# Kernel optimization log

Hardware: AMD Instinct MI355X
Metric: run time of the kernel (lower is better)

## Reference

```python
import jax, jax.numpy as jnp
import numpy as np
import math

B, T, D = 16, 2048, 512
W = 12  # window_size


def setup_inputs() -> dict:
    key = jax.random.key(0)
    ks = jax.random.split(key, 5)
    s = 1.0 / math.sqrt(D)
    x = jax.random.normal(ks[0], (B, T, D), dtype=jnp.float32)
    w_ih = jax.random.uniform(ks[1], (3 * D, D), jnp.float32, -s, s)
    w_hh = jax.random.uniform(ks[2], (3 * D, D), jnp.float32, -s, s)
    b_ih = jax.random.uniform(ks[3], (3 * D,), jnp.float32, -s, s)
    b_hh = jax.random.uniform(ks[4], (3 * D,), jnp.float32, -s, s)
    return {"x": x, "w_ih": w_ih, "w_hh": w_hh, "b_ih": b_ih, "b_hh": b_hh}


def reference(x, w_ih, w_hh, b_ih, b_hh):
    b, t, d = x.shape
    # QK^T scores, scaled
    scores = jnp.einsum('btd,bsd->bts', x, x) / math.sqrt(d)
    # local band mask: allowed where |i-j| <= window_size - 1 (local_ws = 2*W)
    idx = jnp.arange(t)
    band = jnp.abs(idx[:, None] - idx[None, :]) <= (W - 1)
    scores = jnp.where(band[None], scores, -1e9)
    # top-k indices per (batch, timestep), sorted ascending (indices are detached)
    ids = jax.lax.top_k(scores, W)[1]            # [B, T, W]
    ids = jnp.sort(ids, axis=-1)
    # eval-mode temporal subsampling: T//4 evenly spaced timesteps (static)
    tids = np.sort(np.linspace(0, t - 1, t // 4).astype(np.int32))
    ids_sel = ids[:, tids, :]                    # [B, Tq, W]
    # gather local windows: feature[b, j, w] = x[b, ids_sel[b, j, w]]
    feature = jnp.take_along_axis(x[:, None, :, :], ids_sel[..., None], axis=2)  # [B, Tq, W, D]
    tq = feature.shape[1]
    seq = feature.reshape(-1, W, d).transpose(1, 0, 2)  # [W, B*Tq, D]

    def gru_step(h, xt):
        gi = xt @ w_ih.T + b_ih
        gh = h @ w_hh.T + b_hh
        i_r, i_z, i_n = jnp.split(gi, 3, axis=-1)
        h_r, h_z, h_n = jnp.split(gh, 3, axis=-1)
        r = jax.nn.sigmoid(i_r + h_r)
        z = jax.nn.sigmoid(i_z + h_z)
        n = jnp.tanh(i_n + r * h_n)
        h = (1.0 - z) * n + z * h
        return h, None

    h0 = jnp.zeros((seq.shape[1], d), dtype=x.dtype)
    h_final, _ = jax.lax.scan(gru_step, h0, seq)
    return h_final.reshape(b, tq, d)
```

## Files before the change

### kernel.cpp

```cpp
#include <hip/hip_runtime.h>
#include <math.h>

#define BB 16
#define TT 2048
#define DD 512
#define WW 12
#define TQ 512
#define NROWS (BB * TQ)

typedef _Float16 f16;
typedef __attribute__((ext_vector_type(8))) _Float16 f16x8;
typedef __attribute__((ext_vector_type(4))) _Float16 f16x4;
typedef __attribute__((ext_vector_type(4))) float f32x4;

#define MFMA16(a, b, c) __builtin_amdgcn_mfma_f32_16x16x32_f16((a), (b), (c), 0, 0, 0)

#define WS_IDS  0u
#define WS_W16  (512u * 1024u)
#define WS_H16  (4u * 1024u * 1024u)
#define WS_GI   (12u * 1024u * 1024u)
#define WS_X16  (108ull * 1024ull * 1024ull)
#define WS_NEED_X16 (140ull * 1024ull * 1024ull)

#define SEL_BLOCKS 2048
#define W_BLOCKS   1536
#define X_BLOCKS   16384

__device__ __forceinline__ float fsigm(float v) { return 1.0f / (1.0f + __expf(-v)); }
__device__ __forceinline__ float ftanh(float v) {
    float a = fabsf(v);
    float t = __expf(-2.0f * a);
    float r = (1.0f - t) / (1.0f + t);
    return copysignf(r, v);
}

__device__ __forceinline__ f16x8 cvt8(float4 a, float4 b) {
    f16x8 r;
    r[0] = (_Float16)a.x; r[1] = (_Float16)a.y; r[2] = (_Float16)a.z; r[3] = (_Float16)a.w;
    r[4] = (_Float16)b.x; r[5] = (_Float16)b.y; r[6] = (_Float16)b.z; r[7] = (_Float16)b.w;
    return r;
}

__global__ __launch_bounds__(256, 4) void prep_kernel(
    const float* __restrict__ x, int* __restrict__ ids,
    const float* __restrict__ wi, const float* __restrict__ wh,
    f16* __restrict__ w16, f16* __restrict__ x16, int has_x16)
{
    const int bid = blockIdx.x;
    const int tid = threadIdx.x;

    if (bid >= SEL_BLOCKS) {
        int rel = bid - SEL_BLOCKS;
        if (rel < W_BLOCKS) {
            const int PER = 3 * DD * DD / 4;
            int i = rel * 256 + tid;
            float4 v;
            if (i < PER) v = ((const float4*)wi)[i];
            else         v = ((const float4*)wh)[i - PER];
            f16x4 o;
            o[0] = (_Float16)v.x; o[1] = (_Float16)v.y; o[2] = (_Float16)v.z; o[3] = (_Float16)v.w;
            *(f16x4*)(w16 + (size_t)i * 4) = o;
        } else {
            int j = (rel - W_BLOCKS) * 256 + tid;
            float4 v = ((const float4*)x)[j];
            f16x4 o;
            o[0] = (_Float16)v.x; o[1] = (_Float16)v.y; o[2] = (_Float16)v.z; o[3] = (_Float16)v.w;
            *(f16x4*)(x16 + (size_t)j * 4) = o;
        }
        return;
    }

    const int wid = tid >> 6, lane = tid & 63;
    const int swz = (bid & 7) * 256 + (bid >> 3);
    const int n = swz * 4 + wid;
    const int b = n >> 9, qi = n & 511;

    int t = (qi == TQ - 1) ? (TT - 1)
          : (int)((double)qi * ((double)(TT - 1) / (double)(TQ - 1)));
    int j0 = t - (WW - 1); if (j0 < 0) j0 = 0;
    int j1 = t + (WW - 1); if (j1 > TT - 1) j1 = TT - 1;
    const int ncand = j1 - j0 + 1;

    const int c = lane & 3, i = lane >> 2;
    const float* qrow = x + ((size_t)b * TT + t) * DD + i * 4;

    float4 q[8];
#pragma unroll
    for (int it = 0; it < 8; ++it) q[it] = *(const float4*)(qrow + it * 64);

    double sv[6];
#pragma unroll
    for (int r = 0; r < 6; ++r) {
        int cc = r * 4 + c;
        int jr = j0 + cc; if (jr > j1) jr = j1;
        const float* krow = x + ((size_t)b * TT + jr) * DD + i * 4;
        double s0 = 0.0, s1 = 0.0;
#pragma unroll
        for (int it = 0; it < 8; ++it) {
            float4 kv = *(const float4*)(krow + it * 64);
            s0 = fma((double)q[it].x, (double)kv.x, s0);
            s1 = fma((double)q[it].y, (double)kv.y, s1);
            s0 = fma((double)q[it].z, (double)kv.z, s0);
            s1 = fma((double)q[it].w, (double)kv.w, s1);
        }
        sv[r] = s0 + s1;
    }

#pragma unroll
    for (int r = 0; r < 6; ++r) {
        double v = sv[r];
        v += __shfl_xor(v, 4);
        v += __shfl_xor(v, 8);
        v += __shfl_xor(v, 16);
        v += __shfl_xor(v, 32);
        sv[r] = v;
    }

    const int rr = lane >> 2;
    double sj = sv[0];
    sj = (rr == 1) ? sv[1] : sj;
    sj = (rr == 2) ? sv[2] : sj;
    sj = (rr == 3) ? sv[3] : sj;
    sj = (rr == 4) ? sv[4] : sj;
    sj = (rr == 5) ? sv[5] : sj;
    bool valid = lane < ncand;
    if (!valid) sj = -1.0e300;

    int rank = 0;
    for (int kk = 0; kk < 2 * WW - 1; ++kk) {
        if (kk >= ncand) break;
        double bs = __shfl(sj, kk);
        rank += (bs > sj || (bs == sj && kk < lane)) ? 1 : 0;
    }
    bool sel = valid && (rank < WW);
    unsigned long long m = __ballot(sel);
    if (sel) {
        int pos = __popcll(m & ((1ull << lane) - 1ull));
        ids[(size_t)n * WW + pos] = j0 + lane;
    }
}

template<bool X16PATH>
__global__ __launch_bounds__(256, 2) void gi_gemm_kernel(
    const float* __restrict__ x,
    const f16* __restrict__ x16,
    const f16* __restrict__ w16,
    const float* __restrict__ b_ih,
    f16* __restrict__ gi)
{
    __shared__ __align__(16) char sB[2][16 * 1024];
    __shared__ __align__(16) char sX[2][16 * 1024];

    const int tid = threadIdx.x;
    const int lane = tid & 63, wid = tid >> 6;
    const int wm = wid >> 1, wn = wid & 1;
    const int l15 = lane & 15, lhi = lane >> 4;
    const int bid = blockIdx.x;
    const int xcd = bid & 7, idx = bid >> 3;
    const int rb = xcd * 32 + idx / 12;
    const int cb = idx % 12;
    const int row0 = rb * 128, c0 = cb * 128;

    const int slot = lane & 3, lc = lane >> 2;
    const f16* bsrc[4]; int bdst[4];
#pragma unroll
    for (int ii = 0; ii < 4; ++ii) {
        int ch = wid * 4 + ii;
        int half = ch >> 3, cg = ch & 7;
        int col = cg * 16 + lc;
        bsrc[ii] = w16 + ((size_t)(c0 + col) * 512 + half * 32
                          + (size_t)((slot ^ ((col >> 1) & 3)) * 8));
        bdst[ii] = half * 8192 + cg * 1024;
    }

    const f16* x16src[4]; int x16dst[4];
    const float* xps[2]; int xdst[2];
    if (X16PATH) {
        const int xrl = lane >> 2, xslot = lane & 3;
        const int xswz = (xslot ^ ((xrl >> 1) & 3)) * 8;
#pragma unroll
        for (int ii = 0; ii < 4; ++ii) {
            int ch2 = wid * 4 + ii;
            int hh = ch2 >> 3, ch = ch2 & 7;
            x16src[ii] = x16 + ((size_t)(row0 + ch * 16 + xrl) * 512 + hh * 32 + xswz);
            x16dst[ii] = hh * 8192 + ch * 1024;
        }
    } else {
#pragma unroll
        for (int seg = 0; seg < 2; ++seg) {
            int row = seg * 64 + (tid >> 2);
            int chunk = (tid & 3) ^ ((row >> 1) & 3);
            xps[seg] = x + (size_t)(row0 + row) * DD + chunk * 8;
            xdst[seg] = seg * 4096 + tid * 16;
        }
    }

    const int swzo = (lhi ^ ((l15 >> 1) & 3)) * 16;
    const int aBase = (wm * 64 + l15) * 64 + swzo;
    const int bBase = (wn * 64 + l15) * 64 + swzo;

    f32x4 acc[4][4];
#pragma unroll
    for (int mf = 0; mf < 4; ++mf)
#pragma unroll
        for (int nf = 0; nf < 4; ++nf) { f32x4 z = {0.f,0.f,0.f,0.f}; acc[mf][nf] = z; }

    {
#pragma unroll
        for (int ii = 0; ii < 4; ++ii)
            __builtin_amdgcn_global_load_lds(
                (const __attribute__((address_space(1))) unsigned*)bsrc[ii],
                (__attribute__((address_space(3))) unsigned*)(&sB[0][0] + bdst[ii]), 16, 0, 0);
        if (X16PATH) {
#pragma unroll
            for (int ii = 0; ii < 4; ++ii)
                __builtin_amdgcn_global_load_lds(
                    (const __attribute__((address_space(1))) unsigned*)x16src[ii],
                    (__attribute__((address_space(3))) unsigned*)(&sX[0][0] + x16dst[ii]), 16, 0, 0);
        } else {
#pragma unroll
            for (int seg = 0; seg < 2; ++seg)
#pragma unroll
                for (int h = 0; h < 2; ++h) {
                    float4 a0 = *(const float4*)(xps[seg] + h * 32);
                    float4 a1 = *(const float4*)(xps[seg] + h * 32 + 4);
                    *(f16x8*)(&sX[0][0] + h * 8192 + xdst[seg]) = cvt8(a0, a1);
                }
        }
    }

    int cur = 0;
    for (int ks = 0; ks < 8; ++ks) {
        asm volatile("s_waitcnt vmcnt(0)" ::: "memory");
        __syncthreads();

        const int kn = (ks + 1) * 64;
        float4 a[2][2][2];
        if (ks < 7) {
#pragma unroll
            for (int ii = 0; ii < 4; ++ii)
                __builtin_amdgcn_global_load_lds(
                    (const __attribute__((address_space(1))) unsigned*)(bsrc[ii] + kn),
                    (__attribute__((address_space(3))) unsigned*)(&sB[cur ^ 1][0] + bdst[ii]), 16, 0, 0);
            if (X16PATH) {
#pragma unroll
                for (int ii = 0; ii < 4; ++ii)
                    __builtin_amdgcn_global_load_lds(
                        (const __attribute__((address_space(1))) unsigned*)(x16src[ii] + kn),
                        (__attribute__((address_space(3))) unsigned*)(&sX[cur ^ 1][0] + x16dst[ii]), 16, 0, 0);
            } else {
#pragma unroll
                for (int seg = 0; seg < 2; ++seg)
#pragma unroll
                    for (int h = 0; h < 2; ++h) {
                        a[seg][h][0] = *(const float4*)(xps[seg] + kn + h * 32);
                        a[seg][h][1] = *(const float4*)(xps[seg] + kn + h * 32 + 4);
                    }
            }
        }

        __builtin_amdgcn_s_setprio(1);
#pragma unroll
        for (int h = 0; h < 2; ++h) {
            f16x8 ax[4];
#pragma unroll
            for (int mf = 0; mf < 4; ++mf)
                ax[mf] = *(const f16x8*)(&sX[cur][0] + h * 8192 + aBase + mf * 1024);
#pragma unroll
            for (int nf = 0; nf < 4; ++nf) {
                f16x8 Bv = *(const f16x8*)(&sB[cur][0] + h * 8192 + bBase + nf * 1024);
#pragma unroll
                for (int mf = 0; mf < 4; ++mf)
                    acc[mf][nf] = MFMA16(ax[mf], Bv, acc[mf][nf]);
            }
        }
        __builtin_amdgcn_s_setprio(0);

        if (!X16PATH && ks < 7) {
#pragma unroll
            for (int seg = 0; seg < 2; ++seg)
#pragma unroll
                for (int h = 0; h < 2; ++h)
                    *(f16x8*)(&sX[cur ^ 1][0] + h * 8192 + xdst[seg]) = cvt8(a[seg][h][0], a[seg][h][1]);
        }
        cur ^= 1;
    }

#pragma unroll
    for (int nf = 0; nf < 4; ++nf) {
        int col = c0 + wn * 64 + nf * 16 + l15;
        float bi = b_ih[col];
#pragma unroll
        for (int mf = 0; mf < 4; ++mf)
#pragma unroll
            for (int r = 0; r < 4; ++r) {
                int row = row0 + wm * 64 + mf * 16 + lhi * 4 + r;
                gi[(size_t)row * 1536 + col] = (f16)(acc[mf][nf][r] + bi);
            }
    }
}

__global__ __launch_bounds__(256) void step0_kernel(
    const int* __restrict__ ids, const f16* __restrict__ gi,
    const float* __restrict__ b_hh, f16* __restrict__ h16w)
{
    int g = blockIdx.x * 256 + threadIdx.x;
    int row = g >> 6;
    int c8 = (g & 63) * 8;
    int src = (row >> 9) * TT + ids[(size_t)row * WW + 0];
    const f16* gr = gi + (size_t)src * 1536 + c8;
    f16x8 vr = *(const f16x8*)(gr);
    f16x8 vz = *(const f16x8*)(gr + 512);
    f16x8 vn = *(const f16x8*)(gr + 1024);
    f16x8 out;
#pragma unroll
    for (int j = 0; j < 8; ++j) {
        int col = c8 + j;
        float R = fsigm((float)vr[j] + b_hh[col]);
        float Z = fsigm((float)vz[j] + b_hh[DD + col]);
        float N = ftanh((float)vn[j] + R * b_hh[2 * DD + col]);
        out[j] = (f16)((1.0f - Z) * N);
    }
    *(f16x8*)(h16w + (size_t)row * DD + c8) = out;
}

__global__ __launch_bounds__(256, 2) void gru_step_h_kernel(
    const int* __restrict__ ids,
    const f16* __restrict__ w16,
    const float* __restrict__ b_hh,
    const f16* __restrict__ gi,
    const f16* __restrict__ h16r,
    f16* __restrict__ h16w,
    float* __restrict__ f32w,
    int step)
{
    __shared__ __align__(16) char sB[2][24 * 1024];
    __shared__ __align__(16) char sH[2][16 * 1024];

    const int tid = threadIdx.x;
    const int lane = tid & 63, wid = tid >> 6;
    const int wm = wid >> 1, wn = wid & 1;
    const int l15 = lane & 15, lhi = lane >> 4;
    const int bid = blockIdx.x;
    const int xcd = bid & 7, idx = bid >> 3;
    const int rb = xcd * 8 + (idx & 7);
    const int cb = idx >> 3;
    const int row0 = rb * 128, c0 = cb * 64;

    const int lrow = lane >> 3, lslot = lane & 7;
    const int sswz = (lslot ^ lrow) * 8;

    const f16* bsrc[6]; int bdst[6];
#pragma unroll
    for (int ii = 0; ii < 6; ++ii) {
        int ch = wid * 6 + ii;
        int gate = ch >> 3, cg = ch & 7;
        int col = cg * 8 + lrow;
        bsrc[ii] = w16 + ((size_t)(1536 + gate * 512 + c0 + col) * 512 + sswz);
        bdst[ii] = gate * 8192 + cg * 1024 + lrow * 128 + lslot * 16;
    }
    const f16* hsrc[4]; int hdst[4];
#pragma unroll
    for (int ii = 0; ii < 4; ++ii) {
        int ch = wid * 4 + ii;
        int hrow = ch * 8 + lrow;
        hsrc[ii] = h16r + ((size_t)(row0 + hrow) * 512 + sswz);
        hdst[ii] = ch * 1024 + lrow * 128 + lslot * 16;
    }

    const int rowrd = wm * 64 + l15;
    const int colrd = wn * 32 + l15;
    int aOff[4][2], bOff[2][2];
#pragma unroll
    for (int mf = 0; mf < 4; ++mf)
#pragma unroll
        for (int h = 0; h < 2; ++h) {
            int rr2 = rowrd + mf * 16;
            aOff[mf][h] = rr2 * 128 + ((((h << 2) | lhi) ^ (rr2 & 7)) << 4);
        }
#pragma unroll
    for (int nf = 0; nf < 2; ++nf)
#pragma unroll
        for (int h = 0; h < 2; ++h) {
            int cc = colrd + nf * 16;
            bOff[nf][h] = cc * 128 + ((((h << 2) | lhi) ^ (cc & 7)) << 4);
        }

    f32x4 accR[4][2], accZ[4][2], accHN[4][2];
#pragma unroll
    for (int mf = 0; mf < 4; ++mf)
#pragma unroll
        for (int nf = 0; nf < 2; ++nf) {
            f32x4 z = {0.f, 0.f, 0.f, 0.f};
            accR[mf][nf] = z; accZ[mf][nf] = z; accHN[mf][nf] = z;
        }

#pragma unroll
    for (int ii = 0; ii < 6; ++ii)
        __builtin_amdgcn_global_load_lds(
            (const __attribute__((address_space(1))) unsigned*)bsrc[ii],
            (__attribute__((address_space(3))) unsigned*)(&sB[0][0] + bdst[ii]), 16, 0, 0);
#pragma unroll
    for (int ii = 0; ii < 4; ++ii)
        __builtin_amdgcn_global_load_lds(
            (const __attribute__((address_space(1))) unsigned*)hsrc[ii],
            (__attribute__((address_space(3))) unsigned*)(&sH[0][0] + hdst[ii]), 16, 0, 0);

    int cur = 0;
    for (int ks = 0; ks < 8; ++ks) {
        asm volatile("s_waitcnt vmcnt(0)" ::: "memory");
        __syncthreads();

        const int kn = (ks + 1) * 64;
        if (ks < 7) {
#pragma unroll
            for (int ii = 0; ii < 6; ++ii)
                __builtin_amdgcn_global_load_lds(
                    (const __attribute__((address_space(1))) unsigned*)(bsrc[ii] + kn),
                    (__attribute__((address_space(3))) unsigned*)(&sB[cur ^ 1][0] + bdst[ii]), 16, 0, 0);
#pragma unroll
            for (int ii = 0; ii < 4; ++ii)
                __builtin_amdgcn_global_load_lds(
                    (const __attribute__((address_space(1))) unsigned*)(hsrc[ii] + kn),
                    (__attribute__((address_space(3))) unsigned*)(&sH[cur ^ 1][0] + hdst[ii]), 16, 0, 0);
        }

        __builtin_amdgcn_s_setprio(1);
#pragma unroll
        for (int h = 0; h < 2; ++h) {
            f16x8 ah[4];
#pragma unroll
            for (int mf = 0; mf < 4; ++mf)
                ah[mf] = *(const f16x8*)(&sH[cur][0] + aOff[mf][h]);
#pragma unroll
            for (int nf = 0; nf < 2; ++nf) {
                const char* bb = &sB[cur][0] + bOff[nf][h];
                f16x8 B0 = *(const f16x8*)(bb + 0 * 8192);
                f16x8 B1 = *(const f16x8*)(bb + 1 * 8192);
                f16x8 B2 = *(const f16x8*)(bb + 2 * 8192);
#pragma unroll
                for (int mf = 0; mf < 4; ++mf) {
                    accR[mf][nf]  = MFMA16(ah[mf], B0, accR[mf][nf]);
                    accZ[mf][nf]  = MFMA16(ah[mf], B1, accZ[mf][nf]);
                    accHN[mf][nf] = MFMA16(ah[mf], B2, accHN[mf][nf]);
                }
            }
        }
        __builtin_amdgcn_s_setprio(0);
        cur ^= 1;
    }

    float bh[2][3];
#pragma unroll
    for (int nf = 0; nf < 2; ++nf) {
        int col = c0 + wn * 32 + nf * 16 + l15;
        bh[nf][0] = b_hh[col];
        bh[nf][1] = b_hh[DD + col];
        bh[nf][2] = b_hh[2 * DD + col];
    }
#pragma unroll
    for (int mf = 0; mf < 4; ++mf) {
        float g0[2][4], g1[2][4], g2[2][4], hv[2][4];
#pragma unroll
        for (int nf = 0; nf < 2; ++nf) {
            int col = c0 + wn * 32 + nf * 16 + l15;
#pragma unroll
            for (int r = 0; r < 4; ++r) {
                int row = row0 + wm * 64 + mf * 16 + lhi * 4 + r;
                int src = (row >> 9) * TT + ids[(size_t)row * WW + step];
                const f16* gr = gi + (size_t)src * 1536 + col;
                g0[nf][r] = (float)gr[0];
                g1[nf][r] = (float)gr[512];
                g2[nf][r] = (float)gr[1024];
                hv[nf][r] = (float)h16r[(size_t)row * DD + col];
            }
        }
#pragma unroll
        for (int nf = 0; nf < 2; ++nf) {
            int col = c0 + wn * 32 + nf * 16 + l15;
#pragma unroll
            for (int r = 0; r < 4; ++r) {
                int row = row0 + wm * 64 + mf * 16 + lhi * 4 + r;
                size_t off = (size_t)row * DD + col;
                float R = fsigm(g0[nf][r] + accR[mf][nf][r] + bh[nf][0]);
                float Z = fsigm(g1[nf][r] + accZ[mf][nf][r] + bh[nf][1]);
                float N = ftanh(g2[nf][r] + R * (accHN[mf][nf][r] + bh[nf][2]));
                float res = (1.0f - Z) * N + Z * hv[nf][r];
                if (h16w) h16w[off] = (f16)res;
                if (f32w) f32w[off] = res;
            }
        }
    }
}

extern "C" void kernel_launch(void* const* d_in, const int* in_sizes, int n_in,
                              void* d_out, int out_size, void* d_ws, size_t ws_size,
                              hipStream_t stream)
{
    const float* x    = (const float*)d_in[0];
    const float* w_ih = (const float*)d_in[1];
    const float* w_hh = (const float*)d_in[2];
    const float* b_ih = (const float*)d_in[3];
    const float* b_hh = (const float*)d_in[4];

    char* ws = (char*)d_ws;
    int*  ids = (int*)(ws + WS_IDS);
    f16*  w16 = (f16*)(ws + WS_W16);
    f16*  P0  = (f16*)(ws + WS_H16);
    f16*  P1  = (f16*)d_out;
    f16*  gi  = (f16*)(ws + WS_GI);
    float* fo = (float*)d_out;

    const int has_x16 = (ws_size >= WS_NEED_X16) ? 1 : 0;
    f16* x16 = has_x16 ? (f16*)(ws + WS_X16) : nullptr;

    int prep_grid = SEL_BLOCKS + W_BLOCKS + (has_x16 ? X_BLOCKS : 0);
    prep_kernel<<<dim3(prep_grid), dim3(256), 0, stream>>>(
        x, ids, w_ih, w_hh, w16, x16, has_x16);

    if (has_x16)
        gi_gemm_kernel<true><<<dim3(3072), dim3(256), 0, stream>>>(x, x16, w16, b_ih, gi);
    else
        gi_gemm_kernel<false><<<dim3(3072), dim3(256), 0, stream>>>(x, x16, w16, b_ih, gi);

    step0_kernel<<<dim3(2048), dim3(256), 0, stream>>>(ids, gi, b_hh, P0);

    for (int s = 1; s < WW; ++s) {
        const f16* hr = (s & 1) ? P0 : P1;
        f16* hw      = (s == WW - 1) ? nullptr : ((s & 1) ? P1 : P0);
        float* fw    = (s == WW - 1) ? fo : nullptr;
        gru_step_h_kernel<<<dim3(512), dim3(256), 0, stream>>>(
            ids, w16, b_hh, gi, hr, hw, fw, s);
    }
}
```

Before: 427.8 us.

## Fuse GRU recurrent steps into one persistent cooperative kernel with per-row-block flags

Replaces the eleven separate per-step GRU kernel launches with a single cooperative persistent kernel that loops over steps. Blocks that share a 128-row block synchronise through an atomic counter, so there is no grid-wide barrier between steps. Each step's hidden state goes to its own workspace buffer, which avoids write-after-read hazards without a full barrier. The aim is to remove launch overhead and inter-kernel drain between dependent steps. In exchange it needs more workspace, adds a memset and spin-waiting, and depends on cooperative launch succeeding.

```diff
diff --git a/kernel.cpp b/kernel.cpp
--- a/kernel.cpp
+++ b/kernel.cpp
@@ -15,12 +15,16 @@
 
 #define MFMA16(a, b, c) __builtin_amdgcn_mfma_f32_16x16x32_f16((a), (b), (c), 0, 0, 0)
 
-#define WS_IDS  0u
-#define WS_W16  (512u * 1024u)
-#define WS_H16  (4u * 1024u * 1024u)
-#define WS_GI   (12u * 1024u * 1024u)
-#define WS_X16  (108ull * 1024ull * 1024ull)
-#define WS_NEED_X16 (140ull * 1024ull * 1024ull)
+#define WS_IDS   0u
+#define WS_W16   (512u * 1024u)
+#define WS_FLAGS (3584u * 1024u)
+#define WS_P0    (4u * 1024u * 1024u)
+#define WS_GI    (12u * 1024u * 1024u)
+#define WS_X16   (108ull * 1024ull * 1024ull)
+#define WS_P5    (140ull * 1024ull * 1024ull)
+#define WS_NEED_X16     (140ull * 1024ull * 1024ull)
+#define WS_NEED_PERSIST (188ull * 1024ull * 1024ull)
+#define HSZ ((size_t)NROWS * DD)
 
 #define SEL_BLOCKS 2048
 #define W_BLOCKS   1536
@@ -324,67 +328,31 @@
     *(f16x8*)(h16w + (size_t)row * DD + c8) = out;
 }
 
-__global__ __launch_bounds__(256, 2) void gru_step_h_kernel(
-    const int* __restrict__ ids,
-    const f16* __restrict__ w16,
-    const float* __restrict__ b_hh,
-    const f16* __restrict__ gi,
-    const f16* __restrict__ h16r,
-    f16* __restrict__ h16w,
-    float* __restrict__ f32w,
-    int step)
-{
-    __shared__ __align__(16) char sB[2][24 * 1024];
-    __shared__ __align__(16) char sH[2][16 * 1024];
-
-    const int tid = threadIdx.x;
-    const int lane = tid & 63, wid = tid >> 6;
-    const int wm = wid >> 1, wn = wid & 1;
-    const int l15 = lane & 15, lhi = lane >> 4;
-    const int bid = blockIdx.x;
-    const int xcd = bid & 7, idx = bid >> 3;
-    const int rb = xcd * 8 + (idx & 7);
-    const int cb = idx >> 3;
-    const int row0 = rb * 128, c0 = cb * 64;
-
+struct StepPre {
+    const f16* bsrc[6]; int bdst[6];
+    int aOff[4][2], bOff[2][2];
+    int row0, c0, wm, wn, l15, lhi, tid;
+};
+
+__device__ __forceinline__ void gru_body(
+    const StepPre& P, char (*sB)[24 * 1024], char (*sH)[16 * 1024],
+    const int* __restrict__ ids, const float* __restrict__ b_hh,
+    const f16* __restrict__ gi, const f16* __restrict__ h16r,
+    f16* __restrict__ h16w, float* __restrict__ f32w, int step)
+{
+    const int wid = P.tid >> 6;
+    const int lane = P.tid & 63;
     const int lrow = lane >> 3, lslot = lane & 7;
     const int sswz = (lslot ^ lrow) * 8;
 
-    const f16* bsrc[6]; int bdst[6];
-#pragma unroll
-    for (int ii = 0; ii < 6; ++ii) {
-        int ch = wid * 6 + ii;
-        int gate = ch >> 3, cg = ch & 7;
-        int col = cg * 8 + lrow;
-        bsrc[ii] = w16 + ((size_t)(1536 + gate * 512 + c0 + col) * 512 + sswz);
-        bdst[ii] = gate * 8192 + cg * 1024 + lrow * 128 + lslot * 16;
-    }
     const f16* hsrc[4]; int hdst[4];
 #pragma unroll
     for (int ii = 0; ii < 4; ++ii) {
         int ch = wid * 4 + ii;
         int hrow = ch * 8 + lrow;
-        hsrc[ii] = h16r + ((size_t)(row0 + hrow) * 512 + sswz);
+        hsrc[ii] = h16r + ((size_t)(P.row0 + hrow) * 512 + sswz);
         hdst[ii] = ch * 1024 + lrow * 128 + lslot * 16;
     }
-
-    const int rowrd = wm * 64 + l15;
-    const int colrd = wn * 32 + l15;
-    int aOff[4][2], bOff[2][2];
-#pragma unroll
-    for (int mf = 0; mf < 4; ++mf)
-#pragma unroll
-        for (int h = 0; h < 2; ++h) {
-            int rr2 = rowrd + mf * 16;
-            aOff[mf][h] = rr2 * 128 + ((((h << 2) | lhi) ^ (rr2 & 7)) << 4);
-        }
-#pragma unroll
-    for (int nf = 0; nf < 2; ++nf)
-#pragma unroll
-        for (int h = 0; h < 2; ++h) {
-            int cc = colrd + nf * 16;
-            bOff[nf][h] = cc * 128 + ((((h << 2) | lhi) ^ (cc & 7)) << 4);
-        }
 
     f32x4 accR[4][2], accZ[4][2], accHN[4][2];
 #pragma unroll
@@ -398,8 +366,8 @@
 #pragma unroll
     for (int ii = 0; ii < 6; ++ii)
         __builtin_amdgcn_global_load_lds(
-            (const __attribute__((address_space(1))) unsigned*)bsrc[ii],
-            (__attribute__((address_space(3))) unsigned*)(&sB[0][0] + bdst[ii]), 16, 0, 0);
+            (const __attribute__((address_space(1))) unsigned*)P.bsrc[ii],
+            (__attribute__((address_space(3))) unsigned*)(&sB[0][0] + P.bdst[ii]), 16, 0, 0);
 #pragma unroll
     for (int ii = 0; ii < 4; ++ii)
         __builtin_amdgcn_global_load_lds(
@@ -416,8 +384,8 @@
 #pragma unroll
             for (int ii = 0; ii < 6; ++ii)
                 __builtin_amdgcn_global_load_lds(
-                    (const __attribute__((address_space(1))) unsigned*)(bsrc[ii] + kn),
-                    (__attribute__((address_space(3))) unsigned*)(&sB[cur ^ 1][0] + bdst[ii]), 16, 0, 0);
+                    (const __attribute__((address_space(1))) unsigned*)(P.bsrc[ii] + kn),
+                    (__attribute__((address_space(3))) unsigned*)(&sB[cur ^ 1][0] + P.bdst[ii]), 16, 0, 0);
 #pragma unroll
             for (int ii = 0; ii < 4; ++ii)
                 __builtin_amdgcn_global_load_lds(
@@ -431,10 +399,10 @@
             f16x8 ah[4];
 #pragma unroll
             for (int mf = 0; mf < 4; ++mf)
-                ah[mf] = *(const f16x8*)(&sH[cur][0] + aOff[mf][h]);
+                ah[mf] = *(const f16x8*)(&sH[cur][0] + P.aOff[mf][h]);
 #pragma unroll
             for (int nf = 0; nf < 2; ++nf) {
-                const char* bb = &sB[cur][0] + bOff[nf][h];
+                const char* bb = &sB[cur][0] + P.bOff[nf][h];
                 f16x8 B0 = *(const f16x8*)(bb + 0 * 8192);
                 f16x8 B1 = *(const f16x8*)(bb + 1 * 8192);
                 f16x8 B2 = *(const f16x8*)(bb + 2 * 8192);
@@ -453,7 +421,7 @@
     float bh[2][3];
 #pragma unroll
     for (int nf = 0; nf < 2; ++nf) {
-        int col = c0 + wn * 32 + nf * 16 + l15;
+        int col = P.c0 + P.wn * 32 + nf * 16 + P.l15;
         bh[nf][0] = b_hh[col];
         bh[nf][1] = b_hh[DD + col];
         bh[nf][2] = b_hh[2 * DD + col];
@@ -463,10 +431,10 @@
         float g0[2][4], g1[2][4], g2[2][4], hv[2][4];
 #pragma unroll
         for (int nf = 0; nf < 2; ++nf) {
-            int col = c0 + wn * 32 + nf * 16 + l15;
+            int col = P.c0 + P.wn * 32 + nf * 16 + P.l15;
 #pragma unroll
             for (int r = 0; r < 4; ++r) {
-                int row = row0 + wm * 64 + mf * 16 + lhi * 4 + r;
+                int row = P.row0 + P.wm * 64 + mf * 16 + P.lhi * 4 + r;
                 int src = (row >> 9) * TT + ids[(size_t)row * WW + step];
                 const f16* gr = gi + (size_t)src * 1536 + col;
                 g0[nf][r] = (float)gr[0];
@@ -477,10 +445,10 @@
         }
 #pragma unroll
         for (int nf = 0; nf < 2; ++nf) {
-            int col = c0 + wn * 32 + nf * 16 + l15;
+            int col = P.c0 + P.wn * 32 + nf * 16 + P.l15;
 #pragma unroll
             for (int r = 0; r < 4; ++r) {
-                int row = row0 + wm * 64 + mf * 16 + lhi * 4 + r;
+                int row = P.row0 + P.wm * 64 + mf * 16 + P.lhi * 4 + r;
                 size_t off = (size_t)row * DD + col;
                 float R = fsigm(g0[nf][r] + accR[mf][nf][r] + bh[nf][0]);
                 float Z = fsigm(g1[nf][r] + accZ[mf][nf][r] + bh[nf][1]);
@@ -493,6 +461,110 @@
     }
 }
 
+__device__ __forceinline__ void step_pre_init(StepPre& P, const f16* w16)
+{
+    const int tid = P.tid;
+    const int lane = tid & 63, wid = tid >> 6;
+    const int lrow = lane >> 3, lslot = lane & 7;
+    const int sswz = (lslot ^ lrow) * 8;
+#pragma unroll
+    for (int ii = 0; ii < 6; ++ii) {
+        int ch = wid * 6 + ii;
+        int gate = ch >> 3, cg = ch & 7;
+        int col = cg * 8 + lrow;
+        P.bsrc[ii] = w16 + ((size_t)(1536 + gate * 512 + P.c0 + col) * 512 + sswz);
+        P.bdst[ii] = gate * 8192 + cg * 1024 + lrow * 128 + lslot * 16;
+    }
+    const int rowrd = P.wm * 64 + P.l15;
+    const int colrd = P.wn * 32 + P.l15;
+#pragma unroll
+    for (int mf = 0; mf < 4; ++mf)
+#pragma unroll
+        for (int h = 0; h < 2; ++h) {
+            int rr2 = rowrd + mf * 16;
+            P.aOff[mf][h] = rr2 * 128 + ((((h << 2) | P.lhi) ^ (rr2 & 7)) << 4);
+        }
+#pragma unroll
+    for (int nf = 0; nf < 2; ++nf)
+#pragma unroll
+        for (int h = 0; h < 2; ++h) {
+            int cc = colrd + nf * 16;
+            P.bOff[nf][h] = cc * 128 + ((((h << 2) | P.lhi) ^ (cc & 7)) << 4);
+        }
+}
+
+__global__ __launch_bounds__(256, 2) void gru_step_h_kernel(
+    const int* __restrict__ ids, const f16* __restrict__ w16,
+    const float* __restrict__ b_hh, const f16* __restrict__ gi,
+    const f16* __restrict__ h16r, f16* __restrict__ h16w,
+    float* __restrict__ f32w, int step)
+{
+    __shared__ __align__(16) char sB[2][24 * 1024];
+    __shared__ __align__(16) char sH[2][16 * 1024];
+
+    StepPre P;
+    P.tid = threadIdx.x;
+    const int lane = P.tid & 63, wid = P.tid >> 6;
+    P.wm = wid >> 1; P.wn = wid & 1;
+    P.l15 = lane & 15; P.lhi = lane >> 4;
+    const int bid = blockIdx.x;
+    const int xcd = bid & 7, idx = bid >> 3;
+    P.row0 = (xcd * 8 + (idx & 7)) * 128;
+    P.c0 = (idx >> 3) * 64;
+    step_pre_init(P, w16);
+    gru_body(P, sB, sH, ids, b_hh, gi, h16r, h16w, f32w, step);
+}
+
+__global__ __launch_bounds__(256, 2) void gru_steps_persist_kernel(
+    const int* __restrict__ ids, const f16* __restrict__ w16,
+    const float* __restrict__ b_hh, const f16* __restrict__ gi,
+    f16* __restrict__ p0, f16* __restrict__ p14, f16* __restrict__ p5a,
+    float* __restrict__ f32out, unsigned int* __restrict__ cnt)
+{
+    __shared__ __align__(16) char sB[2][24 * 1024];
+    __shared__ __align__(16) char sH[2][16 * 1024];
+
+    StepPre P;
+    P.tid = threadIdx.x;
+    const int lane = P.tid & 63, wid = P.tid >> 6;
+    P.wm = wid >> 1; P.wn = wid & 1;
+    P.l15 = lane & 15; P.lhi = lane >> 4;
+    const int bid = blockIdx.x;
+    const int xcd = bid & 7, idx = bid >> 3;
+    const int rb = xcd * 8 + (idx & 7);
+    P.row0 = rb * 128;
+    P.c0 = (idx >> 3) * 64;
+    step_pre_init(P, w16);
+
+    unsigned int* flag = cnt + rb * 32;
+
+    for (int s = 1; s < WW; ++s) {
+        int pi = s - 1;
+        const f16* hr = (pi == 0) ? p0
+                       : (pi < 5) ? (p14 + (size_t)(pi - 1) * HSZ)
+                                  : (p5a + (size_t)(pi - 5) * HSZ);
+        f16* hw = nullptr; float* fw = nullptr;
+        if (s == WW - 1) fw = f32out;
+        else hw = (s < 5) ? (p14 + (size_t)(s - 1) * HSZ)
+                          : (p5a + (size_t)(s - 5) * HSZ);
+
+        gru_body(P, sB, sH, ids, b_hh, gi, hr, hw, fw, s);
+
+        if (s < WW - 1) {
+            asm volatile("s_waitcnt vmcnt(0)" ::: "memory");
+            __syncthreads();
+            if (P.tid == 0) {
+                __hip_atomic_fetch_add(flag, 1u, __ATOMIC_RELEASE, __HIP_MEMORY_SCOPE_AGENT);
+                unsigned int target = 8u * (unsigned int)s;
+                while (__hip_atomic_load(flag, __ATOMIC_ACQUIRE, __HIP_MEMORY_SCOPE_AGENT) < target)
+                    __builtin_amdgcn_s_sleep(8);
+            }
+            __syncthreads();
+            asm volatile("" ::: "memory");
+        }
+    }
+}
+
 extern "C" void kernel_launch(void* const* d_in, const int* in_sizes, int n_in,
                               void* d_out, int out_size, void* d_ws, size_t ws_size,
                               hipStream_t stream)
@@ -506,12 +578,13 @@
     char* ws = (char*)d_ws;
     int*  ids = (int*)(ws + WS_IDS);
     f16*  w16 = (f16*)(ws + WS_W16);
-    f16*  P0  = (f16*)(ws + WS_H16);
-    f16*  P1  = (f16*)d_out;
+    f16*  P0  = (f16*)(ws + WS_P0);
+    f16*  P1d = (f16*)d_out;
     f16*  gi  = (f16*)(ws + WS_GI);
     float* fo = (float*)d_out;
 
     const int has_x16 = (ws_size >= WS_NEED_X16) ? 1 : 0;
+    const int persist = (ws_size >= WS_NEED_PERSIST) ? 1 : 0;
     f16* x16 = has_x16 ? (f16*)(ws + WS_X16) : nullptr;
 
     int prep_grid = SEL_BLOCKS + W_BLOCKS + (has_x16 ? X_BLOCKS : 0);
@@ -525,11 +598,28 @@
 
     step0_kernel<<<dim3(2048), dim3(256), 0, stream>>>(ids, gi, b_hh, P0);
 
-    for (int s = 1; s < WW; ++s) {
-        const f16* hr = (s & 1) ? P0 : P1;
-        f16* hw      = (s == WW - 1) ? nullptr : ((s & 1) ? P1 : P0);
-        float* fw    = (s == WW - 1) ? fo : nullptr;
-        gru_step_h_kernel<<<dim3(512), dim3(256), 0, stream>>>(
-            ids, w16, b_hh, gi, hr, hw, fw, s);
-    }
-}
+    bool done = false;
+    if (persist) {
+        unsigned int* cnt = (unsigned int*)(ws + WS_FLAGS);
+        hipMemsetAsync(cnt, 0, 64 * 32 * sizeof(unsigned int), stream);
+        f16* p14 = (f16*)(ws + WS_X16);
+        f16* p5a = (f16*)(ws + WS_P5);
+        const int* ids_c = ids; const f16* w16_c = w16; const f16* gi_c = gi;
+        const float* bhh_c = b_hh;
+        void* args[] = { (void*)&ids_c, (void*)&w16_c, (void*)&bhh_c, (void*)&gi_c,
+                         (void*)&P0, (void*)&p14, (void*)&p5a, (void*)&fo, (void*)&cnt };
+        hipError_t err = hipLaunchCooperativeKernel(
+            gru_steps_persist_kernel, dim3(512), dim3(256), args, 0, stream);
+        done = (err == hipSuccess);
+    }
+
+    if (!done) {
+        for (int s = 1; s < WW; ++s) {
+            const f16* hr = (s & 1) ? P0 : P1d;
+            f16* hw      = (s == WW - 1) ? nullptr : ((s & 1) ? P1d : P0);
+            float* fw    = (s == WW - 1) ? fo : nullptr;
+            gru_step_h_kernel<<<dim3(512), dim3(256), 0, stream>>>(
+                ids, w16, b_hh, gi, hr, hw, fw, s);
+        }
+    }
+}
```

Result: slower. 927.4 us (+116.8%).
